# Optimization experiments

Measured on AMD Instinct MI355X. Metric: run time of the kernel, lower is better.

## Reference

```python
import jax, jax.numpy as jnp
import numpy as np

DEPTH, HEADS, DIM_HEAD = 3, 8, 64
DIM = 512
MAX_SEQ = 2048
INNER = HEADS * DIM_HEAD  # 512
FF_HID = 4 * DIM          # 2048
EPS = 1e-5


def sparsemax(z):
    # z: (..., n); sparsemax projection onto the simplex (Martins & Astudillo 2016)
    n = z.shape[-1]
    z_sorted = jnp.flip(jnp.sort(z, axis=-1), axis=-1)            # descending
    cs = jnp.cumsum(z_sorted, axis=-1)
    ks = jnp.arange(1, n + 1, dtype=z.dtype)
    support = 1.0 + ks * z_sorted > cs                            # bool
    k_z = jnp.sum(support, axis=-1, keepdims=True)                # int support size
    cs_k = jnp.take_along_axis(cs, k_z - 1, axis=-1)
    tau = (cs_k - 1.0) / k_z.astype(z.dtype)
    return jnp.maximum(z - tau, 0.0)


def layernorm(x, g, b):
    mu = jnp.mean(x, axis=-1, keepdims=True)
    var = jnp.mean(jnp.square(x - mu), axis=-1, keepdims=True)
    return (x - mu) * jax.lax.rsqrt(var + EPS) * g + b


def setup_inputs() -> dict:
    key = jax.random.key(0)
    ks = jax.random.split(key, 12)
    s = 0.02
    inp = {
        "x": jax.random.normal(ks[0], (8, 1024, DIM), dtype=jnp.float32),
        "proj_w": jax.random.normal(ks[1], (DIM, DIM), dtype=jnp.float32) * s,
        "proj_b": jnp.zeros((DIM,), dtype=jnp.float32),
        "pos_emb": jax.random.normal(ks[2], (MAX_SEQ, DIM), dtype=jnp.float32) * s,
        "ln1_g": jnp.ones((DEPTH, DIM), dtype=jnp.float32),
        "ln1_b": jnp.zeros((DEPTH, DIM), dtype=jnp.float32),
        "wqkv": jax.random.normal(ks[3], (DEPTH, DIM, 3 * INNER), dtype=jnp.float32) * s,
        "wout": jax.random.normal(ks[4], (DEPTH, INNER, DIM), dtype=jnp.float32) * s,
        "bout": jnp.zeros((DEPTH, DIM), dtype=jnp.float32),
        "ln2_g": jnp.ones((DEPTH, DIM), dtype=jnp.float32),
        "ln2_b": jnp.zeros((DEPTH, DIM), dtype=jnp.float32),
        "w1": jax.random.normal(ks[5], (DEPTH, DIM, 2 * FF_HID), dtype=jnp.float32) * s,
        "b1": jnp.zeros((DEPTH, 2 * FF_HID), dtype=jnp.float32),
        "w2": jax.random.normal(ks[6], (DEPTH, FF_HID, DIM), dtype=jnp.float32) * s,
        "b2": jnp.zeros((DEPTH, DIM), dtype=jnp.float32),
    }
    return inp


def reference(x, proj_w, proj_b, pos_emb, ln1_g, ln1_b, wqkv, wout, bout,
              ln2_g, ln2_b, w1, b1, w2, b2):
    B, S, D = x.shape
    scale = DIM_HEAD ** -0.5
    x = x @ proj_w + proj_b                       # projection
    x = x + pos_emb[:S][None, :, :]               # positional embedding
    for l in range(DEPTH):
        # --- attention block (Residual(PreNorm(Attention))) ---
        h = layernorm(x, ln1_g[l], ln1_b[l])
        qkv = h @ wqkv[l]                         # (B,S,3*INNER)
        q, k, v = jnp.split(qkv, 3, axis=-1)
        rs = lambda t: t.reshape(B, S, HEADS, DIM_HEAD).transpose(0, 2, 1, 3)
        q, k, v = rs(q), rs(k), rs(v)             # (B,H,S,Dh)
        sim = jnp.einsum('bhid,bhjd->bhij', q, k) * scale
        attn = sparsemax(sim)
        out = jnp.einsum('bhij,bhjd->bhid', attn, v)
        out = out.transpose(0, 2, 1, 3).reshape(B, S, INNER)
        x = x + (out @ wout[l] + bout[l])
        # --- feedforward block (Residual(PreNorm(GEGLU FFN))) ---
        h = layernorm(x, ln2_g[l], ln2_b[l])
        hh = h @ w1[l] + b1[l]                    # (B,S,2*FF_HID)
        a, g = jnp.split(hh, 2, axis=-1)
        ff = (a * jax.nn.gelu(g, approximate=False)) @ w2[l] + b2[l]
        x = x + ff
    return jnp.mean(x, axis=1)                    # (B, D) mean pool
```

## Files before the change

### kernel.cpp

```cpp
#include <hip/hip_runtime.h>
#include <stdint.h>

typedef unsigned short u16;
typedef __attribute__((ext_vector_type(8))) short short8;
typedef __attribute__((ext_vector_type(4))) float f32x4;

__device__ __forceinline__ float bf2f(u16 u){
  union { unsigned u; float f; } v; v.u = ((unsigned)u) << 16; return v.f;
}
__device__ __forceinline__ u16 f2bf(float f){
  union { float f; unsigned u; } v; v.f = f;
  unsigned u = v.u;
  return (u16)((u + 0x7FFFu + ((u >> 16) & 1u)) >> 16);
}
__device__ __forceinline__ void g2lds16(const u16* g, u16* lds){
  __builtin_amdgcn_global_load_lds(
      (const __attribute__((address_space(1))) unsigned int*)g,
      (__attribute__((address_space(3))) unsigned int*)lds, 16, 0, 0);
}

__global__ void k_flag(const unsigned* __restrict__ ln1g, int* __restrict__ flag){
  if (threadIdx.x == 0 && blockIdx.x == 0)
    *flag = (ln1g[0] == 0x3F800000u) ? 0 : 1;
}

__global__ void k_cvt_f32(const void* __restrict__ src, float* __restrict__ dst, int n,
                          const int* __restrict__ flag){
  int i = blockIdx.x * blockDim.x + threadIdx.x;
  if (i < n) dst[i] = (*flag) ? bf2f(((const u16*)src)[i]) : ((const float*)src)[i];
}
__global__ void k_cvt_bf16(const void* __restrict__ src, u16* __restrict__ dst, int n,
                           const int* __restrict__ flag){
  int i = blockIdx.x * blockDim.x + threadIdx.x;
  if (i < n) dst[i] = (*flag) ? ((const u16*)src)[i] : f2bf(((const float*)src)[i]);
}

__global__ void k_transpose(const void* __restrict__ src, u16* __restrict__ dst,
                            int K, int N, const int* __restrict__ flag){
  __shared__ u16 tile[32][33];
  int n0 = blockIdx.x * 32, k0 = blockIdx.y * 32;
  size_t zsrc = (size_t)blockIdx.z * K * N;
  size_t zdst = (size_t)blockIdx.z * N * K;
  int tx = threadIdx.x & 31, ty = threadIdx.x >> 5;
  bool isbf = (*flag) != 0;
  const float* sf = (const float*)src; const u16* sb = (const u16*)src;
  #pragma unroll
  for (int p = 0; p < 4; ++p){
    int kk = k0 + p*8 + ty, nn = n0 + tx;
    size_t idx = zsrc + (size_t)kk * N + nn;
    tile[tx][p*8+ty] = isbf ? sb[idx] : f2bf(sf[idx]);
  }
  __syncthreads();
  #pragma unroll
  for (int p = 0; p < 4; ++p){
    int nn = n0 + p*8 + ty, kk = k0 + tx;
    dst[zdst + (size_t)nn * K + kk] = tile[p*8+ty][tx];
  }
}

__global__ void k_vt(const u16* __restrict__ src, u16* __restrict__ dst){
  __shared__ u16 tile[32][33];
  int d0 = blockIdx.x * 32, s0 = blockIdx.y * 32;
  size_t base = (size_t)blockIdx.z * 65536;
  int tx = threadIdx.x & 31, ty = threadIdx.x >> 5;
  #pragma unroll
  for (int p = 0; p < 4; ++p)
    tile[tx][p*8+ty] = src[base + (size_t)(s0 + p*8 + ty) * 64 + d0 + tx];
  __syncthreads();
  #pragma unroll
  for (int p = 0; p < 4; ++p)
    dst[base + (size_t)(d0 + p*8 + ty) * 1024 + s0 + tx] = tile[p*8+ty][tx];
}

__global__ __launch_bounds__(256) void k_ln(const float* __restrict__ x,
                                            const float* __restrict__ g,
                                            const float* __restrict__ b,
                                            u16* __restrict__ out){
  int row = blockIdx.x, tid = threadIdx.x;
  const float* xr = x + (size_t)row * 512;
  float x0 = xr[tid], x1 = xr[tid + 256];
  float s = x0 + x1, ss = x0*x0 + x1*x1;
  #pragma unroll
  for (int off = 1; off < 64; off <<= 1){ s += __shfl_xor(s, off, 64); ss += __shfl_xor(ss, off, 64); }
  __shared__ float as_[4], bs_[4];
  int wv = tid >> 6, lane = tid & 63;
  if (lane == 0){ as_[wv] = s; bs_[wv] = ss; }
  __syncthreads();
  s = as_[0] + as_[1] + as_[2] + as_[3];
  ss = bs_[0] + bs_[1] + bs_[2] + bs_[3];
  float mu = s * (1.f/512.f);
  float var = ss * (1.f/512.f) - mu*mu;
  float rs = rsqrtf(var + 1e-5f);
  out[(size_t)row*512 + tid]       = f2bf((x0 - mu) * rs * g[tid]       + b[tid]);
  out[(size_t)row*512 + tid + 256] = f2bf((x1 - mu) * rs * g[tid + 256] + b[tid + 256]);
}

__global__ __launch_bounds__(256) void k_gemm(const u16* __restrict__ A,
                                              const u16* __restrict__ Wt, int K, int mode,
                                              float* __restrict__ xres, u16* __restrict__ out16,
                                              const float* __restrict__ bias,
                                              const float* __restrict__ pos){
  __shared__ u16 As[128*64];
  __shared__ u16 Bs[128*64];
  const int tid = threadIdx.x;
  const int wv = tid >> 6, lane = tid & 63;
  const int lm = lane & 15, lq = lane >> 4;
  const int wm = (wv >> 1) * 64, wn = (wv & 1) * 64;
  const int m0 = blockIdx.y * 128, n0 = blockIdx.x * 128;
  const int lrow = lane >> 3;
  const int scol = ((lane & 7) ^ lrow) << 3;
  f32x4 acc[4][4];
  #pragma unroll
  for (int i = 0; i < 4; ++i)
    #pragma unroll
    for (int j = 0; j < 4; ++j){ f32x4 z = {0.f,0.f,0.f,0.f}; acc[i][j] = z; }

  for (int k0 = 0; k0 < K; k0 += 64){
    #pragma unroll
    for (int it = 0; it < 4; ++it){
      int ci = wv*4 + it;
      int row = ci*8 + lrow;
      g2lds16(&A [(size_t)(m0 + row) * K + k0 + scol], &As[ci*512]);
      g2lds16(&Wt[(size_t)(n0 + row) * K + k0 + scol], &Bs[ci*512]);
    }
    __syncthreads();
    #pragma unroll
    for (int kk = 0; kk < 2; ++kk){
      short8 af[4], bf[4];
      #pragma unroll
      for (int t = 0; t < 4; ++t){
        int cs = ((kk*4 + lq) ^ (lm & 7)) << 3;
        af[t] = *(const short8*)&As[(wm + t*16 + lm)*64 + cs];
        bf[t] = *(const short8*)&Bs[(wn + t*16 + lm)*64 + cs];
      }
      #pragma unroll
      for (int i = 0; i < 4; ++i)
        #pragma unroll
        for (int j = 0; j < 4; ++j)
          acc[i][j] = __builtin_amdgcn_mfma_f32_16x16x32_bf16(af[i], bf[j], acc[i][j], 0, 0, 0);
    }
    __syncthreads();
  }
  #pragma unroll
  for (int i = 0; i < 4; ++i)
    #pragma unroll
    for (int j = 0; j < 4; ++j)
      #pragma unroll
      for (int r = 0; r < 4; ++r){
        int row = m0 + wm + i*16 + lq*4 + r;
        int col = n0 + wn + j*16 + lm;
        float v = acc[i][j][r];
        if (mode == 0){
          xres[(size_t)row*512 + col] = v + bias[col] + pos[(size_t)(row & 1023)*512 + col];
        } else if (mode == 1){
          int part = col >> 9, within = col & 511;
          int head = within >> 6, dh = within & 63;
          int b = row >> 10, s = row & 1023;
          out16[(size_t)part*4194304 + (((size_t)(b*8 + head)*1024 + s) << 6) + dh] = f2bf(v);
        } else {
          size_t idx = (size_t)row*512 + col;
          xres[idx] = xres[idx] + v + bias[col];
        }
      }
}

__global__ __launch_bounds__(256) void k_gemm64(const u16* __restrict__ A,
                                                const u16* __restrict__ Wt, int K, int mode,
                                                float* __restrict__ xres,
                                                const float* __restrict__ bias,
                                                const float* __restrict__ pos){
  __shared__ u16 As[64*64];
  __shared__ u16 Bs[128*64];
  const int tid = threadIdx.x;
  const int wv = tid >> 6, lane = tid & 63;
  const int lm = lane & 15, lq = lane >> 4;
  const int wm = (wv >> 1) * 32, wn = (wv & 1) * 64;
  const int m0 = blockIdx.y * 64, n0 = blockIdx.x * 128;
  const int lrow = lane >> 3;
  const int scol = ((lane & 7) ^ lrow) << 3;
  f32x4 acc[2][4];
  #pragma unroll
  for (int i = 0; i < 2; ++i)
    #pragma unroll
    for (int j = 0; j < 4; ++j){ f32x4 z = {0.f,0.f,0.f,0.f}; acc[i][j] = z; }

  for (int k0 = 0; k0 < K; k0 += 64){
    #pragma unroll
    for (int it = 0; it < 2; ++it){
      int ci = wv*2 + it;
      int row = ci*8 + lrow;
      g2lds16(&A[(size_t)(m0 + row) * K + k0 + scol], &As[ci*512]);
    }
    #pragma unroll
    for (int it = 0; it < 4; ++it){
      int ci = wv*4 + it;
      int row = ci*8 + lrow;
      g2lds16(&Wt[(size_t)(n0 + row) * K + k0 + scol], &Bs[ci*512]);
    }
    __syncthreads();
    #pragma unroll
    for (int kk = 0; kk < 2; ++kk){
      short8 af[2], bf[4];
      int cs = ((kk*4 + lq) ^ (lm & 7)) << 3;
      #pragma unroll
      for (int t = 0; t < 2; ++t)
        af[t] = *(const short8*)&As[(wm + t*16 + lm)*64 + cs];
      #pragma unroll
      for (int t = 0; t < 4; ++t)
        bf[t] = *(const short8*)&Bs[(wn + t*16 + lm)*64 + cs];
      #pragma unroll
      for (int i = 0; i < 2; ++i)
        #pragma unroll
        for (int j = 0; j < 4; ++j)
          acc[i][j] = __builtin_amdgcn_mfma_f32_16x16x32_bf16(af[i], bf[j], acc[i][j], 0, 0, 0);
    }
    __syncthreads();
  }
  #pragma unroll
  for (int i = 0; i < 2; ++i)
    #pragma unroll
    for (int j = 0; j < 4; ++j)
      #pragma unroll
      for (int r = 0; r < 4; ++r){
        int row = m0 + wm + i*16 + lq*4 + r;
        int col = n0 + wn + j*16 + lm;
        float v = acc[i][j][r];
        if (mode == 0){
          xres[(size_t)row*512 + col] = v + bias[col] + pos[(size_t)(row & 1023)*512 + col];
        } else {
          size_t idx = (size_t)row*512 + col;
          xres[idx] = xres[idx] + v + bias[col];
        }
      }
}

__global__ __launch_bounds__(256) void k_ff1_geglu64(const u16* __restrict__ A,
                                                     const u16* __restrict__ W1t,
                                                     const float* __restrict__ b1,
                                                     u16* __restrict__ ffh){
  __shared__ u16 As[64*64];
  __shared__ u16 Ba[128*64];
  __shared__ u16 Bg[128*64];
  const int tid = threadIdx.x;
  const int wv = tid >> 6, lane = tid & 63;
  const int lm = lane & 15, lq = lane >> 4;
  const int wm = (wv >> 1) * 32, wn = (wv & 1) * 64;
  const int m0 = blockIdx.y * 64, n0 = blockIdx.x * 128;
  const int lrow = lane >> 3;
  const int scol = ((lane & 7) ^ lrow) << 3;
  const int K = 512;
  f32x4 aa[2][4], ag[2][4];
  #pragma unroll
  for (int i = 0; i < 2; ++i)
    #pragma unroll
    for (int j = 0; j < 4; ++j){ f32x4 z = {0.f,0.f,0.f,0.f}; aa[i][j] = z; ag[i][j] = z; }
  for (int k0 = 0; k0 < K; k0 += 64){
    #pragma unroll
    for (int it = 0; it < 2; ++it){
      int ci = wv*2 + it;
      int row = ci*8 + lrow;
      g2lds16(&A[(size_t)(m0 + row) * K + k0 + scol], &As[ci*512]);
    }
    #pragma unroll
    for (int it = 0; it < 4; ++it){
      int ci = wv*4 + it;
      int row = ci*8 + lrow;
      g2lds16(&W1t[(size_t)(n0 + row) * K + k0 + scol],        &Ba[ci*512]);
      g2lds16(&W1t[(size_t)(2048 + n0 + row) * K + k0 + scol], &Bg[ci*512]);
    }
    __syncthreads();
    #pragma unroll
    for (int kk = 0; kk < 2; ++kk){
      short8 af[2], ba[4], bg[4];
      int cs = ((kk*4 + lq) ^ (lm & 7)) << 3;
      #pragma unroll
      for (int t = 0; t < 2; ++t)
        af[t] = *(const short8*)&As[(wm + t*16 + lm)*64 + cs];
      #pragma unroll
      for (int t = 0; t < 4; ++t){
        ba[t] = *(const short8*)&Ba[(wn + t*16 + lm)*64 + cs];
        bg[t] = *(const short8*)&Bg[(wn + t*16 + lm)*64 + cs];
      }
      #pragma unroll
      for (int i = 0; i < 2; ++i)
        #pragma unroll
        for (int j = 0; j < 4; ++j){
          aa[i][j] = __builtin_amdgcn_mfma_f32_16x16x32_bf16(af[i], ba[j], aa[i][j], 0, 0, 0);
          ag[i][j] = __builtin_amdgcn_mfma_f32_16x16x32_bf16(af[i], bg[j], ag[i][j], 0, 0, 0);
        }
    }
    __syncthreads();
  }
  #pragma unroll
  for (int i = 0; i < 2; ++i)
    #pragma unroll
    for (int j = 0; j < 4; ++j)
      #pragma unroll
      for (int r = 0; r < 4; ++r){
        int row = m0 + wm + i*16 + lq*4 + r;
        int n = n0 + wn + j*16 + lm;
        float a = aa[i][j][r] + b1[n];
        float g = ag[i][j][r] + b1[2048 + n];
        float ge = 0.5f * g * (1.0f + erff(g * 0.70710678118654752440f));
        ffh[(size_t)row*2048 + n] = f2bf(a * ge);
      }
}

__global__ __launch_bounds__(256) void k_qkspmax(const u16* __restrict__ qb,
                                                 const u16* __restrict__ kb,
                                                 u16* __restrict__ P, int bh0){
  __shared__ u16 Qs[4][32*64];
  __shared__ u16 Ks[4][64*64];
  __shared__ float red_s[4][32];
  __shared__ float red_c[4][32];
  __shared__ float tauL[32];
  __shared__ int flagL;
  const int tid = threadIdx.x;
  const int wv = tid >> 6, lane = tid & 63;
  const int lm = lane & 15, lq = lane >> 4;
  const int lrow = lane >> 3, c8 = lane & 7;
  const int m0 = blockIdx.x * 32;
  const size_t base = (size_t)(bh0 + blockIdx.y) * 65536;
  const size_t pb = (size_t)blockIdx.y * 1048576;

  #pragma unroll
  for (int it = 0; it < 4; ++it){
    int row = it*8 + lrow;
    g2lds16(&qb[base + (size_t)(m0 + row) * 64 + ((c8 ^ (row & 7)) << 3)], &Qs[wv][it*512]);
  }
  f32x4 acc[4][2][4];
  #pragma unroll
  for (int kt = 0; kt < 4; ++kt)
    #pragma unroll
    for (int i = 0; i < 2; ++i)
      #pragma unroll
      for (int j = 0; j < 4; ++j){ f32x4 z = {0.f,0.f,0.f,0.f}; acc[kt][i][j] = z; }

  for (int kt = 0; kt < 4; ++kt){
    if (kt) __builtin_amdgcn_s_waitcnt(0);
    int kbase = (wv*4 + kt) * 64;
    #pragma unroll
    for (int it = 0; it < 8; ++it){
      int row = it*8 + lrow;
      g2lds16(&kb[base + (size_t)(kbase + row) * 64 + ((c8 ^ (row & 7)) << 3)], &Ks[wv][it*512]);
    }
    __builtin_amdgcn_s_waitcnt(0);
    #pragma unroll
    for (int kk = 0; kk < 2; ++kk){
      int cs = ((kk*4 + lq) ^ (lm & 7)) << 3;
      short8 af[2], bf[4];
      #pragma unroll
      for (int t = 0; t < 2; ++t) af[t] = *(const short8*)&Qs[wv][(t*16 + lm)*64 + cs];
      #pragma unroll
      for (int t = 0; t < 4; ++t) bf[t] = *(const short8*)&Ks[wv][(t*16 + lm)*64 + cs];
      #pragma unroll
      for (int i = 0; i < 2; ++i)
        #pragma unroll
        for (int j = 0; j < 4; ++j)
          acc[kt][i][j] = __builtin_amdgcn_mfma_f32_16x16x32_bf16(af[i], bf[j], acc[kt][i][j], 0, 0, 0);
    }
  }
  #pragma unroll
  for (int kt = 0; kt < 4; ++kt)
    #pragma unroll
    for (int i = 0; i < 2; ++i)
      #pragma unroll
      for (int j = 0; j < 4; ++j)
        #pragma unroll
        for (int r = 0; r < 4; ++r)
          acc[kt][i][j][r] *= 0.125f;

  float tauRow[8];
  #pragma unroll
  for (int i = 0; i < 8; ++i) tauRow[i] = -3.0e38f;
  float myPrevC = -1.f;
  for (int iter = 0; iter < 64; ++iter){
    #pragma unroll
    for (int mt = 0; mt < 2; ++mt)
      #pragma unroll
      for (int r = 0; r < 4; ++r){
        float t = tauRow[mt*4 + r];
        float s = 0.f, c = 0.f;
        #pragma unroll
        for (int kt = 0; kt < 4; ++kt)
          #pragma unroll
          for (int j = 0; j < 4; ++j){
            float zv = acc[kt][mt][j][r];
            if (zv > t){ s += zv; c += 1.f; }
          }
        #pragma unroll
        for (int off = 1; off < 16; off <<= 1){
          s += __shfl_xor(s, off, 64); c += __shfl_xor(c, off, 64);
        }
        if (lm == 0){
          int row = mt*16 + lq*4 + r;
          red_s[wv][row] = s; red_c[wv][row] = c;
        }
      }
    __syncthreads();
    if (wv == 0){
      bool conv = true;
      if (lane < 32){
        float S = red_s[0][lane] + red_s[1][lane] + red_s[2][lane] + red_s[3][lane];
        float C = red_c[0][lane] + red_c[1][lane] + red_c[2][lane] + red_c[3][lane];
        tauL[lane] = (S - 1.0f) / C;
        conv = (C == myPrevC);
        myPrevC = C;
      }
      unsigned long long msk = __ballot(conv);
      if (lane == 0) flagL = (msk == ~0ull) ? 1 : 0;
    }
    __syncthreads();
    #pragma unroll
    for (int mt = 0; mt < 2; ++mt)
      #pragma unroll
      for (int r = 0; r < 4; ++r)
        tauRow[mt*4 + r] = tauL[mt*16 + lq*4 + r];
    if (flagL) break;
  }
  #pragma unroll
  for (int kt = 0; kt < 4; ++kt)
    #pragma unroll
    for (int mt = 0; mt < 2; ++mt)
      #pragma unroll
      for (int j = 0; j < 4; ++j)
        #pragma unroll
        for (int r = 0; r < 4; ++r){
          float p = acc[kt][mt][j][r] - tauRow[mt*4 + r];
          p = p > 0.f ? p : 0.f;
          int row = m0 + mt*16 + lq*4 + r;
          int col = wv*256 + kt*64 + j*16 + lm;
          P[pb + (size_t)row*1024 + col] = f2bf(p);
        }
}

__global__ __launch_bounds__(256) void k_pv(const u16* __restrict__ P,
                                            const u16* __restrict__ vt,
                                            u16* __restrict__ aout, int bh0){
  __shared__ u16 As[64*64];
  __shared__ u16 Bs[64*64];
  const int tid = threadIdx.x;
  const int wv = tid >> 6, lane = tid & 63;
  const int lm = lane & 15, lq = lane >> 4;
  const int m0 = blockIdx.x * 64;
  const int bh = bh0 + blockIdx.y;
  const size_t pbase = (size_t)blockIdx.y * 1048576;
  const size_t vbase = (size_t)bh * 65536;
  const int lrow = lane >> 3;
  const int scol = ((lane & 7) ^ lrow) << 3;
  f32x4 acc[4];
  #pragma unroll
  for (int j = 0; j < 4; ++j){ f32x4 z = {0.f,0.f,0.f,0.f}; acc[j] = z; }

  for (int k0 = 0; k0 < 1024; k0 += 64){
    #pragma unroll
    for (int it = 0; it < 2; ++it){
      int ci = wv*2 + it;
      int row = ci*8 + lrow;
      g2lds16(&P [pbase + (size_t)(m0 + row) * 1024 + k0 + scol], &As[ci*512]);
      g2lds16(&vt[vbase + (size_t)row * 1024 + k0 + scol],        &Bs[ci*512]);
    }
    __syncthreads();
    #pragma unroll
    for (int kk = 0; kk < 2; ++kk){
      int csa = ((kk*4 + lq) ^ (lm & 7)) << 3;
      short8 af = *(const short8*)&As[(wv*16 + lm)*64 + csa];
      #pragma unroll
      for (int j = 0; j < 4; ++j){
        short8 bf = *(const short8*)&Bs[(j*16 + lm)*64 + csa];
        acc[j] = __builtin_amdgcn_mfma_f32_16x16x32_bf16(af, bf, acc[j], 0, 0, 0);
      }
    }
    __syncthreads();
  }
  int b = bh >> 3, h = bh & 7;
  #pragma unroll
  for (int j = 0; j < 4; ++j)
    #pragma unroll
    for (int r = 0; r < 4; ++r){
      int s = m0 + wv*16 + lq*4 + r;
      int d = j*16 + lm;
      aout[((size_t)(b*1024 + s))*512 + h*64 + d] = f2bf(acc[j][r]);
    }
}

__global__ __launch_bounds__(256) void k_attn(const u16* __restrict__ qb,
                                              const u16* __restrict__ kb,
                                              const u16* __restrict__ vb,
                                              u16* __restrict__ aout){
  extern __shared__ char smem[];
  float* sc = (float*)smem;
  u16*  P   = (u16*)smem;
  u16*  Qs  = (u16*)(smem + 131072);
  u16*  KVs = (u16*)(smem + 131072 + 4608);
  const int tid = threadIdx.x;
  const int wv = tid >> 6, lane = tid & 63;
  const int lm = lane & 15, lq = lane >> 4;
  const int bh = blockIdx.y, s0 = blockIdx.x * 32;
  const size_t base = (size_t)bh * 65536;
  {
    int r = tid >> 3, c = tid & 7;
    *(uint4*)&Qs[r*72 + (c << 3)] = *(const uint4*)&qb[base + (size_t)(s0 + r)*64 + (c << 3)];
  }
  for (int kt = 0; kt < 16; ++kt){
    __syncthreads();
    #pragma unroll
    for (int it = 0; it < 2; ++it){
      int s = it*256 + tid; int r = s >> 3, c = s & 7;
      *(uint4*)&KVs[r*72 + (c << 3)] =
          *(const uint4*)&kb[base + (size_t)(kt*64 + r)*64 + (c << 3)];
    }
    __syncthreads();
    f32x4 accs[2];
    { f32x4 z = {0.f,0.f,0.f,0.f}; accs[0] = z; accs[1] = z; }
    #pragma unroll
    for (int kk = 0; kk < 2; ++kk){
      short8 bfk = *(const short8*)&KVs[(wv*16 + lm)*72 + kk*32 + lq*8];
      #pragma unroll
      for (int mt = 0; mt < 2; ++mt){
        short8 af = *(const short8*)&Qs[(mt*16 + lm)*72 + kk*32 + lq*8];
        accs[mt] = __builtin_amdgcn_mfma_f32_16x16x32_bf16(af, bfk, accs[mt], 0, 0, 0);
      }
    }
    #pragma unroll
    for (int mt = 0; mt < 2; ++mt)
      #pragma unroll
      for (int r = 0; r < 4; ++r){
        int row = mt*16 + lq*4 + r;
        int col = kt*64 + wv*16 + lm;
        sc[row*1024 + (((col >> 2) ^ (row & 7)) << 2) + (col & 3)] = accs[mt][r] * 0.125f;
      }
  }
  __syncthreads();
  for (int rr = 0; rr < 8; ++rr){
    int row = wv*8 + rr;
    float z[16];
    #pragma unroll
    for (int i = 0; i < 16; ++i){
      int col = lane + (i << 6);
      z[i] = sc[row*1024 + (((col >> 2) ^ (row & 7)) << 2) + (col & 3)];
    }
    bool act[16];
    #pragma unroll
    for (int i = 0; i < 16; ++i) act[i] = true;
    float prevc = -1.f, tau = 0.f;
    for (int it = 0; it < 64; ++it){
      float s = 0.f, c = 0.f;
      #pragma unroll
      for (int i = 0; i < 16; ++i) if (act[i]){ s += z[i]; c += 1.f; }
      #pragma unroll
      for (int off = 1; off < 64; off <<= 1){ s += __shfl_xor(s, off, 64); c += __shfl_xor(c, off, 64); }
      tau = (s - 1.0f) / c;
      if (c == prevc) break;
      prevc = c;
      #pragma unroll
      for (int i = 0; i < 16; ++i) act[i] = z[i] > tau;
    }
    #pragma unroll
    for (int i = 0; i < 16; ++i){
      int col = lane + (i << 6);
      float p = z[i] - tau; p = p > 0.f ? p : 0.f;
      P[row*2048 + (((col >> 3) ^ (row & 7)) << 3) + (col & 7)] = f2bf(p);
    }
  }
  f32x4 acco[2];
  { f32x4 z = {0.f,0.f,0.f,0.f}; acco[0] = z; acco[1] = z; }
  for (int kt = 0; kt < 16; ++kt){
    __syncthreads();
    {
      int dc = tid >> 6, key = tid & 63;
      const u16* src = &vb[base + (size_t)(kt*64 + key)*64 + dc*16];
      u16 tmp[16];
      *(uint4*)tmp       = *(const uint4*)src;
      *(uint4*)(tmp + 8) = *(const uint4*)(src + 8);
      #pragma unroll
      for (int j = 0; j < 16; ++j) KVs[(dc*16 + j)*72 + key] = tmp[j];
    }
    __syncthreads();
    #pragma unroll
    for (int kk = 0; kk < 2; ++kk){
      short8 bfv = *(const short8*)&KVs[(wv*16 + lm)*72 + kk*32 + lq*8];
      #pragma unroll
      for (int mt = 0; mt < 2; ++mt){
        int m = mt*16 + lm;
        int k = kt*64 + kk*32 + lq*8;
        short8 af = *(const short8*)&P[m*2048 + (((k >> 3) ^ (m & 7)) << 3)];
        acco[mt] = __builtin_amdgcn_mfma_f32_16x16x32_bf16(af, bfv, acco[mt], 0, 0, 0);
      }
    }
  }
  int b = bh >> 3, h = bh & 7;
  #pragma unroll
  for (int mt = 0; mt < 2; ++mt)
    #pragma unroll
    for (int r = 0; r < 4; ++r){
      int row = mt*16 + lq*4 + r;
      int s = s0 + row;
      aout[((size_t)(b*1024 + s))*512 + h*64 + wv*16 + lm] = f2bf(acco[mt][r]);
    }
}

__global__ __launch_bounds__(256) void k_pool1(const float* __restrict__ xres,
                                               float* __restrict__ part){
  int b = blockIdx.y, ch = blockIdx.x, tid = threadIdx.x;
  float a0 = 0.f, a1 = 0.f;
  for (int i = 0; i < 64; ++i){
    const float* r = xres + ((size_t)(b*1024 + ch*64 + i)) * 512;
    a0 += r[tid]; a1 += r[tid + 256];
  }
  part[((size_t)(b*16 + ch))*512 + tid]       = a0;
  part[((size_t)(b*16 + ch))*512 + tid + 256] = a1;
}
__global__ __launch_bounds__(512) void k_pool2(const float* __restrict__ part,
                                               void* __restrict__ out,
                                               const int* __restrict__ flag){
  int b = blockIdx.x, d = threadIdx.x;
  float s = 0.f;
  for (int c = 0; c < 16; ++c) s += part[((size_t)(b*16 + c))*512 + d];
  s *= (1.0f/1024.0f);
  if (*flag) ((u16*)out)[b*512 + d] = f2bf(s);
  else       ((float*)out)[b*512 + d] = s;
}

extern "C" void kernel_launch(void* const* d_in, const int* in_sizes, int n_in,
                              void* d_out, int out_size, void* d_ws, size_t ws_size,
                              hipStream_t stream){
  (void)in_sizes; (void)n_in; (void)out_size;
  char* w = (char*)d_ws;
  size_t off = 0;
  auto alloc = [&](size_t bytes) -> char* {
    char* p = w + off;
    off += (bytes + 255) & ~(size_t)255;
    return p;
  };
  int*   flag  = (int*)  alloc(4);
  float* xres  = (float*)alloc((size_t)8192*512*4);
  u16*   hb    = (u16*)  alloc((size_t)8192*512*2);
  u16*   qb    = (u16*)  alloc((size_t)8388608);
  u16*   kb    = (u16*)  alloc((size_t)8388608);
  u16*   vb    = (u16*)  alloc((size_t)8388608);
  u16*   aoutb = (u16*)  alloc((size_t)8388608);
  u16*   ffh   = qb;
  u16*   pwT   = (u16*)  alloc((size_t)512*512*2);
  u16*   wqkvT = (u16*)  alloc((size_t)3*1536*512*2);
  u16*   woutT = (u16*)  alloc((size_t)3*512*512*2);
  u16*   w1T   = (u16*)  alloc((size_t)3*4096*512*2);
  u16*   w2T   = (u16*)  alloc((size_t)3*512*2048*2);
  float* posf  = (float*)alloc((size_t)1024*512*4);
  float* pbf   = (float*)alloc(512*4);
  float* ln1gf = (float*)alloc(1536*4);
  float* ln1bf = (float*)alloc(1536*4);
  float* ln2gf = (float*)alloc(1536*4);
  float* ln2bf = (float*)alloc(1536*4);
  float* boutf = (float*)alloc(1536*4);
  float* b1f   = (float*)alloc(12288*4);
  float* b2f   = (float*)alloc(1536*4);
  float* part  = (float*)alloc((size_t)8*16*512*4);
  u16*   vt    = (u16*)  alloc((size_t)8388608);

  int chunk = 0;
  u16* Pbuf = nullptr;
  {
    size_t rem = (ws_size > off) ? (ws_size - off) : 0;
    for (int c = 64; c >= 8; c >>= 1){
      size_t need = (size_t)c * 1048576 * 2 + 512;
      if (need <= rem){
        Pbuf = (u16*)alloc((size_t)c * 1048576 * 2);
        chunk = c;
        break;
      }
    }
  }

  const void* x_raw = d_in[0];  const void* projw = d_in[1];  const void* projb = d_in[2];
  const void* pose  = d_in[3];  const void* ln1g  = d_in[4];  const void* ln1b  = d_in[5];
  const void* wqkv  = d_in[6];  const void* wout  = d_in[7];  const void* bout  = d_in[8];
  const void* ln2g  = d_in[9];  const void* ln2b  = d_in[10]; const void* w1    = d_in[11];
  const void* b1    = d_in[12]; const void* w2    = d_in[13]; const void* b2    = d_in[14];

  k_flag<<<1, 1, 0, stream>>>((const unsigned*)ln1g, flag);

  k_transpose<<<dim3(16, 16, 1), 256, 0, stream>>>(projw, pwT,   512,  512, flag);
  k_transpose<<<dim3(48, 16, 3), 256, 0, stream>>>(wqkv,  wqkvT, 512, 1536, flag);
  k_transpose<<<dim3(16, 16, 3), 256, 0, stream>>>(wout,  woutT, 512,  512, flag);
  k_transpose<<<dim3(128,16, 3), 256, 0, stream>>>(w1,    w1T,   512, 4096, flag);
  k_transpose<<<dim3(16, 64, 3), 256, 0, stream>>>(w2,    w2T,  2048,  512, flag);

  k_cvt_f32<<<2,    256, 0, stream>>>(projb, pbf,    512,    flag);
  k_cvt_f32<<<2048, 256, 0, stream>>>(pose,  posf,   524288, flag);
  k_cvt_f32<<<6,    256, 0, stream>>>(ln1g,  ln1gf,  1536,   flag);
  k_cvt_f32<<<6,    256, 0, stream>>>(ln1b,  ln1bf,  1536,   flag);
  k_cvt_f32<<<6,    256, 0, stream>>>(ln2g,  ln2gf,  1536,   flag);
  k_cvt_f32<<<6,    256, 0, stream>>>(ln2b,  ln2bf,  1536,   flag);
  k_cvt_f32<<<6,    256, 0, stream>>>(bout,  boutf,  1536,   flag);
  k_cvt_f32<<<48,   256, 0, stream>>>(b1,    b1f,    12288,  flag);
  k_cvt_f32<<<6,    256, 0, stream>>>(b2,    b2f,    1536,   flag);
  k_cvt_bf16<<<16384, 256, 0, stream>>>(x_raw, hb, 4194304, flag);

  k_gemm64<<<dim3(4, 128), 256, 0, stream>>>(hb, pwT, 512, 0, xres, pbf, posf);

  for (int l = 0; l < 3; ++l){
    k_ln<<<8192, 256, 0, stream>>>(xres, ln1gf + l*512, ln1bf + l*512, hb);
    k_gemm<<<dim3(12, 64), 256, 0, stream>>>(hb, wqkvT + (size_t)l*1536*512, 512, 1,
                                             nullptr, qb, nullptr, nullptr);
    if (chunk){
      k_vt<<<dim3(2, 32, 64), 256, 0, stream>>>(vb, vt);
      for (int bh0 = 0; bh0 < 64; bh0 += chunk){
        k_qkspmax<<<dim3(32, chunk), 256, 0, stream>>>(qb, kb, Pbuf, bh0);
        k_pv<<<dim3(16, chunk), 256, 0, stream>>>(Pbuf, vt, aoutb, bh0);
      }
    } else {
      k_attn<<<dim3(32, 64), 256, 144896, stream>>>(qb, kb, vb, aoutb);
    }
    k_gemm64<<<dim3(4, 128), 256, 0, stream>>>(aoutb, woutT + (size_t)l*512*512, 512, 2,
                                               xres, boutf + l*512, nullptr);
    k_ln<<<8192, 256, 0, stream>>>(xres, ln2gf + l*512, ln2bf + l*512, hb);
    k_ff1_geglu64<<<dim3(16, 128), 256, 0, stream>>>(hb, w1T + (size_t)l*4096*512,
                                                     b1f + l*4096, ffh);
    k_gemm64<<<dim3(4, 128), 256, 0, stream>>>(ffh, w2T + (size_t)l*512*2048, 2048, 2,
                                               xres, b2f + l*512, nullptr);
  }
  k_pool1<<<dim3(16, 8), 256, 0, stream>>>(xres, part);
  k_pool2<<<8, 512, 0, stream>>>(part, d_out, flag);
}
```

Measured before the change: 1.237 ms.

## Rework sparsemax attention per-wave, fuse V transpose into QKV store, vectorize layernorm, fast GELU

Several unrelated changes land together. The QK+sparsemax kernel now has each wave own 16 full query rows and keep all 1024 scores in registers, so the threshold search is a per-wave Newton-style iteration started from the mean, with no LDS reductions or block barriers. The QKV GEMM now writes V already transposed, which removes the separate transpose kernel. Layernorm processes one row per wave with vectorized loads and stores, and the exact erf GELU is replaced by a tanh-style sigmoid approximation, which changes numerics slightly. The register-resident score tile (64 f32x4 accumulators per lane) risks heavy register pressure or spills, and the bound of 48 iterations may not cover every row.

```diff
diff --git a/kernel.cpp b/kernel.cpp
--- a/kernel.cpp
+++ b/kernel.cpp
@@ -17,6 +17,10 @@
   __builtin_amdgcn_global_load_lds(
       (const __attribute__((address_space(1))) unsigned int*)g,
       (__attribute__((address_space(3))) unsigned int*)lds, 16, 0, 0);
+}
+__device__ __forceinline__ float gelu_fast(float g){
+  float u2 = g * (1.5957691216057308f + 0.0713548162726f * g * g);
+  return g * __builtin_amdgcn_rcpf(1.0f + __expf(-u2));
 }
 
 __global__ void k_flag(const unsigned* __restrict__ ln1g, int* __restrict__ flag){
@@ -58,41 +62,32 @@
   }
 }
 
-__global__ void k_vt(const u16* __restrict__ src, u16* __restrict__ dst){
-  __shared__ u16 tile[32][33];
-  int d0 = blockIdx.x * 32, s0 = blockIdx.y * 32;
-  size_t base = (size_t)blockIdx.z * 65536;
-  int tx = threadIdx.x & 31, ty = threadIdx.x >> 5;
-  #pragma unroll
-  for (int p = 0; p < 4; ++p)
-    tile[tx][p*8+ty] = src[base + (size_t)(s0 + p*8 + ty) * 64 + d0 + tx];
-  __syncthreads();
-  #pragma unroll
-  for (int p = 0; p < 4; ++p)
-    dst[base + (size_t)(d0 + p*8 + ty) * 1024 + s0 + tx] = tile[p*8+ty][tx];
-}
-
 __global__ __launch_bounds__(256) void k_ln(const float* __restrict__ x,
                                             const float* __restrict__ g,
                                             const float* __restrict__ b,
                                             u16* __restrict__ out){
-  int row = blockIdx.x, tid = threadIdx.x;
-  const float* xr = x + (size_t)row * 512;
-  float x0 = xr[tid], x1 = xr[tid + 256];
-  float s = x0 + x1, ss = x0*x0 + x1*x1;
+  int wv = threadIdx.x >> 6, lane = threadIdx.x & 63;
+  int row = blockIdx.x * 4 + wv;
+  const float* xr = x + (size_t)row * 512 + lane * 8;
+  float4 v0 = *(const float4*)xr;
+  float4 v1 = *(const float4*)(xr + 4);
+  float s  = v0.x+v0.y+v0.z+v0.w + v1.x+v1.y+v1.z+v1.w;
+  float ss = v0.x*v0.x+v0.y*v0.y+v0.z*v0.z+v0.w*v0.w
+           + v1.x*v1.x+v1.y*v1.y+v1.z*v1.z+v1.w*v1.w;
   #pragma unroll
   for (int off = 1; off < 64; off <<= 1){ s += __shfl_xor(s, off, 64); ss += __shfl_xor(ss, off, 64); }
-  __shared__ float as_[4], bs_[4];
-  int wv = tid >> 6, lane = tid & 63;
-  if (lane == 0){ as_[wv] = s; bs_[wv] = ss; }
-  __syncthreads();
-  s = as_[0] + as_[1] + as_[2] + as_[3];
-  ss = bs_[0] + bs_[1] + bs_[2] + bs_[3];
   float mu = s * (1.f/512.f);
   float var = ss * (1.f/512.f) - mu*mu;
   float rs = rsqrtf(var + 1e-5f);
-  out[(size_t)row*512 + tid]       = f2bf((x0 - mu) * rs * g[tid]       + b[tid]);
-  out[(size_t)row*512 + tid + 256] = f2bf((x1 - mu) * rs * g[tid + 256] + b[tid + 256]);
+  const float* gp = g + lane*8; const float* bp = b + lane*8;
+  float4 g0 = *(const float4*)gp, g1 = *(const float4*)(gp+4);
+  float4 b0 = *(const float4*)bp, b1 = *(const float4*)(bp+4);
+  u16 o[8];
+  o[0]=f2bf((v0.x-mu)*rs*g0.x+b0.x); o[1]=f2bf((v0.y-mu)*rs*g0.y+b0.y);
+  o[2]=f2bf((v0.z-mu)*rs*g0.z+b0.z); o[3]=f2bf((v0.w-mu)*rs*g0.w+b0.w);
+  o[4]=f2bf((v1.x-mu)*rs*g1.x+b1.x); o[5]=f2bf((v1.y-mu)*rs*g1.y+b1.y);
+  o[6]=f2bf((v1.z-mu)*rs*g1.z+b1.z); o[7]=f2bf((v1.w-mu)*rs*g1.w+b1.w);
+  *(uint4*)(out + (size_t)row*512 + lane*8) = *(const uint4*)o;
 }
 
 __global__ __launch_bounds__(256) void k_gemm(const u16* __restrict__ A,
@@ -156,7 +151,11 @@
           int part = col >> 9, within = col & 511;
           int head = within >> 6, dh = within & 63;
           int b = row >> 10, s = row & 1023;
-          out16[(size_t)part*4194304 + (((size_t)(b*8 + head)*1024 + s) << 6) + dh] = f2bf(v);
+          int bh = b*8 + head;
+          size_t o;
+          if (part < 2) o = (size_t)part*4194304 + (((size_t)bh*1024 + s) << 6) + dh;
+          else          o = (size_t)8388608 + (size_t)bh*65536 + (size_t)dh*1024 + s;
+          out16[o] = f2bf(v);
         } else {
           size_t idx = (size_t)row*512 + col;
           xres[idx] = xres[idx] + v + bias[col];
@@ -301,137 +300,96 @@
         int n = n0 + wn + j*16 + lm;
         float a = aa[i][j][r] + b1[n];
         float g = ag[i][j][r] + b1[2048 + n];
-        float ge = 0.5f * g * (1.0f + erff(g * 0.70710678118654752440f));
-        ffh[(size_t)row*2048 + n] = f2bf(a * ge);
-      }
-}
-
-__global__ __launch_bounds__(256) void k_qkspmax(const u16* __restrict__ qb,
-                                                 const u16* __restrict__ kb,
-                                                 u16* __restrict__ P, int bh0){
-  __shared__ u16 Qs[4][32*64];
-  __shared__ u16 Ks[4][64*64];
-  __shared__ float red_s[4][32];
-  __shared__ float red_c[4][32];
-  __shared__ float tauL[32];
-  __shared__ int flagL;
+        ffh[(size_t)row*2048 + n] = f2bf(a * gelu_fast(g));
+      }
+}
+
+__global__ __launch_bounds__(256, 1) void k_qks(const u16* __restrict__ qb,
+                                                const u16* __restrict__ kb,
+                                                u16* __restrict__ P, int bh0){
+  __shared__ u16 Qs[4][1024];
+  __shared__ u16 Ks[4][4096];
   const int tid = threadIdx.x;
   const int wv = tid >> 6, lane = tid & 63;
   const int lm = lane & 15, lq = lane >> 4;
   const int lrow = lane >> 3, c8 = lane & 7;
-  const int m0 = blockIdx.x * 32;
+  const int scol = (c8 ^ lrow) << 3;
+  const int m0 = blockIdx.x * 64 + wv * 16;
   const size_t base = (size_t)(bh0 + blockIdx.y) * 65536;
   const size_t pb = (size_t)blockIdx.y * 1048576;
 
   #pragma unroll
-  for (int it = 0; it < 4; ++it){
+  for (int it = 0; it < 2; ++it){
     int row = it*8 + lrow;
-    g2lds16(&qb[base + (size_t)(m0 + row) * 64 + ((c8 ^ (row & 7)) << 3)], &Qs[wv][it*512]);
-  }
-  f32x4 acc[4][2][4];
-  #pragma unroll
-  for (int kt = 0; kt < 4; ++kt)
-    #pragma unroll
-    for (int i = 0; i < 2; ++i)
-      #pragma unroll
-      for (int j = 0; j < 4; ++j){ f32x4 z = {0.f,0.f,0.f,0.f}; acc[kt][i][j] = z; }
-
-  for (int kt = 0; kt < 4; ++kt){
-    if (kt) __builtin_amdgcn_s_waitcnt(0);
-    int kbase = (wv*4 + kt) * 64;
+    g2lds16(&qb[base + (size_t)(m0 + row) * 64 + scol], &Qs[wv][it*512]);
+  }
+  f32x4 acc[64];
+  #pragma unroll
+  for (int t = 0; t < 64; ++t){ f32x4 z = {0.f,0.f,0.f,0.f}; acc[t] = z; }
+
+  for (int kt = 0; kt < 16; ++kt){
     #pragma unroll
     for (int it = 0; it < 8; ++it){
-      int row = it*8 + lrow;
-      g2lds16(&kb[base + (size_t)(kbase + row) * 64 + ((c8 ^ (row & 7)) << 3)], &Ks[wv][it*512]);
+      int key = kt*64 + it*8 + lrow;
+      g2lds16(&kb[base + (size_t)key * 64 + scol], &Ks[wv][it*512]);
     }
     __builtin_amdgcn_s_waitcnt(0);
     #pragma unroll
     for (int kk = 0; kk < 2; ++kk){
       int cs = ((kk*4 + lq) ^ (lm & 7)) << 3;
-      short8 af[2], bf[4];
-      #pragma unroll
-      for (int t = 0; t < 2; ++t) af[t] = *(const short8*)&Qs[wv][(t*16 + lm)*64 + cs];
-      #pragma unroll
-      for (int t = 0; t < 4; ++t) bf[t] = *(const short8*)&Ks[wv][(t*16 + lm)*64 + cs];
-      #pragma unroll
-      for (int i = 0; i < 2; ++i)
-        #pragma unroll
-        for (int j = 0; j < 4; ++j)
-          acc[kt][i][j] = __builtin_amdgcn_mfma_f32_16x16x32_bf16(af[i], bf[j], acc[kt][i][j], 0, 0, 0);
-    }
-  }
-  #pragma unroll
-  for (int kt = 0; kt < 4; ++kt)
-    #pragma unroll
-    for (int i = 0; i < 2; ++i)
-      #pragma unroll
-      for (int j = 0; j < 4; ++j)
-        #pragma unroll
-        for (int r = 0; r < 4; ++r)
-          acc[kt][i][j][r] *= 0.125f;
-
-  float tauRow[8];
-  #pragma unroll
-  for (int i = 0; i < 8; ++i) tauRow[i] = -3.0e38f;
-  float myPrevC = -1.f;
-  for (int iter = 0; iter < 64; ++iter){
-    #pragma unroll
-    for (int mt = 0; mt < 2; ++mt)
-      #pragma unroll
-      for (int r = 0; r < 4; ++r){
-        float t = tauRow[mt*4 + r];
-        float s = 0.f, c = 0.f;
-        #pragma unroll
-        for (int kt = 0; kt < 4; ++kt)
-          #pragma unroll
-          for (int j = 0; j < 4; ++j){
-            float zv = acc[kt][mt][j][r];
-            if (zv > t){ s += zv; c += 1.f; }
-          }
-        #pragma unroll
-        for (int off = 1; off < 16; off <<= 1){
-          s += __shfl_xor(s, off, 64); c += __shfl_xor(c, off, 64);
-        }
-        if (lm == 0){
-          int row = mt*16 + lq*4 + r;
-          red_s[wv][row] = s; red_c[wv][row] = c;
-        }
-      }
-    __syncthreads();
-    if (wv == 0){
-      bool conv = true;
-      if (lane < 32){
-        float S = red_s[0][lane] + red_s[1][lane] + red_s[2][lane] + red_s[3][lane];
-        float C = red_c[0][lane] + red_c[1][lane] + red_c[2][lane] + red_c[3][lane];
-        tauL[lane] = (S - 1.0f) / C;
-        conv = (C == myPrevC);
-        myPrevC = C;
-      }
-      unsigned long long msk = __ballot(conv);
-      if (lane == 0) flagL = (msk == ~0ull) ? 1 : 0;
-    }
-    __syncthreads();
-    #pragma unroll
-    for (int mt = 0; mt < 2; ++mt)
-      #pragma unroll
-      for (int r = 0; r < 4; ++r)
-        tauRow[mt*4 + r] = tauL[mt*16 + lq*4 + r];
-    if (flagL) break;
-  }
-  #pragma unroll
-  for (int kt = 0; kt < 4; ++kt)
-    #pragma unroll
-    for (int mt = 0; mt < 2; ++mt)
-      #pragma unroll
-      for (int j = 0; j < 4; ++j)
-        #pragma unroll
-        for (int r = 0; r < 4; ++r){
-          float p = acc[kt][mt][j][r] - tauRow[mt*4 + r];
-          p = p > 0.f ? p : 0.f;
-          int row = m0 + mt*16 + lq*4 + r;
-          int col = wv*256 + kt*64 + j*16 + lm;
-          P[pb + (size_t)row*1024 + col] = f2bf(p);
-        }
+      short8 af = *(const short8*)&Qs[wv][lm*64 + cs];
+      #pragma unroll
+      for (int t = 0; t < 4; ++t){
+        short8 bf = *(const short8*)&Ks[wv][(t*16 + lm)*64 + cs];
+        acc[kt*4 + t] = __builtin_amdgcn_mfma_f32_16x16x32_bf16(af, bf, acc[kt*4 + t], 0, 0, 0);
+      }
+    }
+  }
+  #pragma unroll
+  for (int t = 0; t < 64; ++t){
+    acc[t][0] *= 0.125f; acc[t][1] *= 0.125f; acc[t][2] *= 0.125f; acc[t][3] *= 0.125f;
+  }
+  float tau[4], prevc[4];
+  #pragma unroll
+  for (int r = 0; r < 4; ++r){
+    float s = 0.f;
+    #pragma unroll
+    for (int t = 0; t < 64; ++t) s += acc[t][r];
+    #pragma unroll
+    for (int off = 1; off < 16; off <<= 1) s += __shfl_xor(s, off, 64);
+    tau[r] = (s - 1.0f) * (1.0f/1024.0f);
+    prevc[r] = 1024.f;
+  }
+  for (int iter = 0; iter < 48; ++iter){
+    bool conv = true;
+    #pragma unroll
+    for (int r = 0; r < 4; ++r){
+      float s = 0.f, c = 0.f;
+      #pragma unroll
+      for (int t = 0; t < 64; ++t){
+        float p = acc[t][r] - tau[r];
+        if (p > 0.f){ s += p; c += 1.f; }
+      }
+      #pragma unroll
+      for (int off = 1; off < 16; off <<= 1){
+        s += __shfl_xor(s, off, 64); c += __shfl_xor(c, off, 64);
+      }
+      tau[r] += (s - 1.0f) / c;
+      conv = conv && (c == prevc[r]);
+      prevc[r] = c;
+    }
+    if (__ballot(conv) == ~0ull) break;
+  }
+  #pragma unroll
+  for (int t = 0; t < 64; ++t)
+    #pragma unroll
+    for (int r = 0; r < 4; ++r){
+      float p = acc[t][r] - tau[r];
+      p = p > 0.f ? p : 0.f;
+      int row = m0 + lq*4 + r;
+      int col = t*16 + lm;
+      P[pb + (size_t)row*1024 + col] = f2bf(p);
+    }
 }
 
 __global__ __launch_bounds__(256) void k_pv(const u16* __restrict__ P,
@@ -486,7 +444,7 @@
 
 __global__ __launch_bounds__(256) void k_attn(const u16* __restrict__ qb,
                                               const u16* __restrict__ kb,
-                                              const u16* __restrict__ vb,
+                                              const u16* __restrict__ vt,
                                               u16* __restrict__ aout){
   extern __shared__ char smem[];
   float* sc = (float*)smem;
@@ -569,12 +527,9 @@
     __syncthreads();
     {
       int dc = tid >> 6, key = tid & 63;
-      const u16* src = &vb[base + (size_t)(kt*64 + key)*64 + dc*16];
-      u16 tmp[16];
-      *(uint4*)tmp       = *(const uint4*)src;
-      *(uint4*)(tmp + 8) = *(const uint4*)(src + 8);
-      #pragma unroll
-      for (int j = 0; j < 16; ++j) KVs[(dc*16 + j)*72 + key] = tmp[j];
+      #pragma unroll
+      for (int j = 0; j < 16; ++j)
+        KVs[(dc*16 + j)*72 + key] = vt[base + (size_t)(dc*16 + j)*1024 + kt*64 + key];
     }
     __syncthreads();
     #pragma unroll
@@ -638,7 +593,7 @@
   u16*   hb    = (u16*)  alloc((size_t)8192*512*2);
   u16*   qb    = (u16*)  alloc((size_t)8388608);
   u16*   kb    = (u16*)  alloc((size_t)8388608);
-  u16*   vb    = (u16*)  alloc((size_t)8388608);
+  u16*   vtb   = (u16*)  alloc((size_t)8388608);
   u16*   aoutb = (u16*)  alloc((size_t)8388608);
   u16*   ffh   = qb;
   u16*   pwT   = (u16*)  alloc((size_t)512*512*2);
@@ -656,7 +611,6 @@
   float* b1f   = (float*)alloc(12288*4);
   float* b2f   = (float*)alloc(1536*4);
   float* part  = (float*)alloc((size_t)8*16*512*4);
-  u16*   vt    = (u16*)  alloc((size_t)8388608);
 
   int chunk = 0;
   u16* Pbuf = nullptr;
@@ -700,21 +654,20 @@
   k_gemm64<<<dim3(4, 128), 256, 0, stream>>>(hb, pwT, 512, 0, xres, pbf, posf);
 
   for (int l = 0; l < 3; ++l){
-    k_ln<<<8192, 256, 0, stream>>>(xres, ln1gf + l*512, ln1bf + l*512, hb);
+    k_ln<<<2048, 256, 0, stream>>>(xres, ln1gf + l*512, ln1bf + l*512, hb);
     k_gemm<<<dim3(12, 64), 256, 0, stream>>>(hb, wqkvT + (size_t)l*1536*512, 512, 1,
                                              nullptr, qb, nullptr, nullptr);
     if (chunk){
-      k_vt<<<dim3(2, 32, 64), 256, 0, stream>>>(vb, vt);
       for (int bh0 = 0; bh0 < 64; bh0 += chunk){
-        k_qkspmax<<<dim3(32, chunk), 256, 0, stream>>>(qb, kb, Pbuf, bh0);
-        k_pv<<<dim3(16, chunk), 256, 0, stream>>>(Pbuf, vt, aoutb, bh0);
+        k_qks<<<dim3(16, chunk), 256, 0, stream>>>(qb, kb, Pbuf, bh0);
+        k_pv<<<dim3(16, chunk), 256, 0, stream>>>(Pbuf, vtb, aoutb, bh0);
       }
     } else {
-      k_attn<<<dim3(32, 64), 256, 144896, stream>>>(qb, kb, vb, aoutb);
+      k_attn<<<dim3(32, 64), 256, 144896, stream>>>(qb, kb, vtb, aoutb);
     }
     k_gemm64<<<dim3(4, 128), 256, 0, stream>>>(aoutb, woutT + (size_t)l*512*512, 512, 2,
                                                xres, boutf + l*512, nullptr);
-    k_ln<<<8192, 256, 0, stream>>>(xres, ln2gf + l*512, ln2bf + l*512, hb);
+    k_ln<<<2048, 256, 0, stream>>>(xres, ln2gf + l*512, ln2bf + l*512, hb);
     k_ff1_geglu64<<<dim3(16, 128), 256, 0, stream>>>(hb, w1T + (size_t)l*4096*512,
                                                      b1f + l*4096, ffh);
     k_gemm64<<<dim3(4, 128), 256, 0, stream>>>(ffh, w2T + (size_t)l*512*2048, 2048, 2,
```

Result: slower. 1.965 ms (+58.9%).
